# Kernel optimization log

Hardware: AMD Instinct MI355X
Metric: run time of the kernel (lower is better)

The kernel has to match this reference:

```python
import jax, jax.numpy as jnp
import numpy as np

TEMP_POS = 5.0
TEMP_NEG = 10.0
MAX_NEG = 64  # original subsamples at most 64 negatives per row via randperm


def setup_inputs() -> dict:
    key = jax.random.key(0)
    k1, k2 = jax.random.split(key)
    hidden_vectors = jax.random.normal(k1, (1024, 512), dtype=jnp.float32)
    labels = jax.random.randint(k2, (1024,), 0, 2, dtype=jnp.int32)
    return {"hidden_vectors": hidden_vectors, "labels": labels}


def reference(hidden_vectors, labels):
    f32 = hidden_vectors.dtype
    n = hidden_vectors.shape[0]
    # L2-normalize rows, cosine similarity matrix
    h = hidden_vectors / jnp.linalg.norm(hidden_vectors, axis=1, keepdims=True)
    sim = h @ h.T  # (N, N)

    eq = labels[:, None] == labels[None, :]
    eye = jnp.eye(n, dtype=bool)
    mask_pos = eq & ~eye          # same label, not self
    mask_neg = ~eq                # different label

    # Random subsample of up to MAX_NEG negatives per row (Gumbel-free: uniform
    # scores on negative slots, -inf elsewhere, take top-k => uniform random subset).
    noise = jax.random.uniform(jax.random.key(1), (n, n))
    scores = jnp.where(mask_neg, noise, -jnp.inf)
    _, neg_idx = jax.lax.top_k(scores, MAX_NEG)                 # (N, K)
    neg_valid = jnp.take_along_axis(mask_neg, neg_idx, axis=1)  # (N, K) bool
    neg_sim = jnp.take_along_axis(sim, neg_idx, axis=1) / TEMP_NEG  # (N, K)

    pos_sim = sim / TEMP_POS  # (N, N), masked by mask_pos below

    # -log(e^a / (e^a + e^b)) = softplus(b - a)
    pair = jax.nn.softplus(neg_sim[:, None, :] - pos_sim[:, :, None])  # (N, N, K)
    w = mask_pos.astype(f32)[:, :, None] * neg_valid.astype(f32)[:, None, :]
    row_sum = jnp.sum(pair * w, axis=(1, 2))                    # (N,)

    n_pos = jnp.sum(mask_pos, axis=1)
    n_neg = jnp.sum(neg_valid, axis=1)
    n_pairs = (n_pos * n_neg).astype(f32)
    has_pos = n_pos > 0
    row_loss = jnp.where(has_pos, row_sum / jnp.maximum(n_pairs, 1.0), 0.0)

    count = jnp.sum(has_pos).astype(f32)
    return jnp.where(count > 0, jnp.sum(row_loss) / jnp.maximum(count, 1.0), 0.0)
```

## Files before the change

### kernel.cpp

```cpp
#include <hip/hip_runtime.h>
#include <hip/hip_bf16.h>
#include <math.h>
#include <stdint.h>

#define N 1024
#define D 512
#define MAXNEG 64
#define HALF_CNT (1u << 19)

typedef __attribute__((ext_vector_type(8))) short short8;
typedef __attribute__((ext_vector_type(4))) float f32x4;

__device__ __forceinline__ uint32_t rotl32(uint32_t x, uint32_t r) {
    return (x << r) | (x >> (32u - r));
}

__device__ __forceinline__ uint2 tf_pair(uint32_t f) {
    const uint32_t K0 = 0u, K1 = 1u;
    const uint32_t KS2 = 0x1BD11BDBu;
    uint32_t x0 = f, x1 = f + HALF_CNT;
    x0 += K0; x1 += K1;
#define TFR(r) { x0 += x1; x1 = rotl32(x1, (r)); x1 ^= x0; }
    TFR(13) TFR(15) TFR(26) TFR(6)
    x0 += K1;  x1 += KS2 + 1u;
    TFR(17) TFR(29) TFR(16) TFR(24)
    x0 += KS2; x1 += K0 + 2u;
    TFR(13) TFR(15) TFR(26) TFR(6)
    x0 += K0;  x1 += K1 + 3u;
    TFR(17) TFR(29) TFR(16) TFR(24)
    x0 += K1;  x1 += KS2 + 4u;
    TFR(13) TFR(15) TFR(26) TFR(6)
    x0 += KS2; x1 += K0 + 5u;
#undef TFR
    return make_uint2(x0, x1);
}

__device__ __forceinline__ unsigned long long shflx_u64(unsigned long long v, int m) {
    unsigned lo = (unsigned)(v & 0xffffffffull);
    unsigned hi = (unsigned)(v >> 32);
    lo = __shfl_xor(lo, m, 64);
    hi = __shfl_xor(hi, m, 64);
    return ((unsigned long long)hi << 32) | (unsigned long long)lo;
}

__device__ __forceinline__ ushort f2bf(float x) {
    __hip_bfloat16 h = __float2bfloat16(x);
    return *(ushort*)&h;
}

__global__ __launch_bounds__(256) void k_norms(const float* __restrict__ V,
                                               float* __restrict__ inv,
                                               ushort* __restrict__ Vh,
                                               float* __restrict__ gsum,
                                               float* __restrict__ gcnt,
                                               unsigned* __restrict__ done) {
    if (blockIdx.x == 0 && threadIdx.x == 0) { *gsum = 0.0f; *gcnt = 0.0f; *done = 0u; }
    const int w = threadIdx.x >> 6, l = threadIdx.x & 63;
    const int r = blockIdx.x * 4 + w;
    const float4* vp = (const float4*)(V + (size_t)r * D);
    float4 a = vp[l], b = vp[l + 64];
    float ss = a.x*a.x + a.y*a.y + a.z*a.z + a.w*a.w
             + b.x*b.x + b.y*b.y + b.z*b.z + b.w*b.w;
#pragma unroll
    for (int off = 32; off > 0; off >>= 1) ss += __shfl_xor(ss, off, 64);
    if (l == 0) inv[r] = 1.0f / sqrtf(ss);
    ushort4 ua, ub;
    ua.x = f2bf(a.x); ua.y = f2bf(a.y); ua.z = f2bf(a.z); ua.w = f2bf(a.w);
    ub.x = f2bf(b.x); ub.y = f2bf(b.y); ub.z = f2bf(b.z); ub.w = f2bf(b.w);
    *(ushort4*)(Vh + (size_t)r * D + 4 * l)       = ua;
    *(ushort4*)(Vh + (size_t)r * D + 256 + 4 * l) = ub;
}

__global__ __launch_bounds__(64) void k_gemm(const ushort* __restrict__ Vh,
                                             float* __restrict__ sim) {
    const int l  = threadIdx.x;
    const int bi = blockIdx.y, bj = blockIdx.x;
    const int lr = l & 15, lk = (l >> 4) * 8;

    const ushort* Ab = Vh + (size_t)(bi * 64 + lr) * D + lk;
    const ushort* Bb = Vh + (size_t)(bj * 64 + lr) * D + lk;

    f32x4 acc[4][4];
#pragma unroll
    for (int m = 0; m < 4; ++m)
#pragma unroll
        for (int n = 0; n < 4; ++n) acc[m][n] = (f32x4){0.f, 0.f, 0.f, 0.f};

    short8 a[4], b[4], na[4], nb[4];
#pragma unroll
    for (int m = 0; m < 4; ++m) a[m] = *(const short8*)(Ab + (size_t)m * 16 * D);
#pragma unroll
    for (int n = 0; n < 4; ++n) b[n] = *(const short8*)(Bb + (size_t)n * 16 * D);

    for (int k0 = 32; k0 <= D; k0 += 32) {
        if (k0 < D) {
#pragma unroll
            for (int m = 0; m < 4; ++m) na[m] = *(const short8*)(Ab + (size_t)m * 16 * D + k0);
#pragma unroll
            for (int n = 0; n < 4; ++n) nb[n] = *(const short8*)(Bb + (size_t)n * 16 * D + k0);
        }
#pragma unroll
        for (int m = 0; m < 4; ++m)
#pragma unroll
            for (int n = 0; n < 4; ++n)
                acc[m][n] = __builtin_amdgcn_mfma_f32_16x16x32_bf16(a[m], b[n], acc[m][n], 0, 0, 0);
        if (k0 < D) {
#pragma unroll
            for (int m = 0; m < 4; ++m) a[m] = na[m];
#pragma unroll
            for (int n = 0; n < 4; ++n) b[n] = nb[n];
        }
    }

    const int r0 = (l >> 4) * 4;
#pragma unroll
    for (int m = 0; m < 4; ++m) {
#pragma unroll
        for (int r = 0; r < 4; ++r) {
            float* dst = sim + (size_t)(bi * 64 + m * 16 + r0 + r) * N + bj * 64 + lr;
#pragma unroll
            for (int n = 0; n < 4; ++n) dst[n * 16] = acc[m][n][r];
        }
    }
}

__global__ __launch_bounds__(256) void k_rowloss(const float* __restrict__ sim,
                                                 const float* __restrict__ inv,
                                                 const int* __restrict__ labels,
                                                 float* __restrict__ gsum,
                                                 float* __restrict__ gcnt,
                                                 unsigned* __restrict__ done,
                                                 float* __restrict__ out) {
    __shared__ __align__(16) float simrow0[N];
    __shared__ __align__(16) float simrow1[N];
    __shared__ int   hist0[256], hist1[256];
    __shared__ unsigned long long list0[256], list1[256];
    __shared__ float ens0[MAXNEG], ens1[MAXNEG];
    __shared__ int   wpart0[4], wpart1[4];
    __shared__ float wsA[4], wsB[4];
    __shared__ int   wpA[4], wpB[4];
    __shared__ int   s_B0, s_r0, s_cnt0, s_lcnt0;
    __shared__ int   s_B1, s_r1, s_cnt1, s_lcnt1;

    const int b = blockIdx.x;
    const int i0 = b, i1 = b + 512;
    const int t = threadIdx.x;
    const int lane = t & 63, w = t >> 6;
    const int jb = t * 4;

    if (t == 0) {
        s_B0 = -1; s_r0 = 0; s_cnt0 = 0; s_lcnt0 = 0;
        s_B1 = -1; s_r1 = 0; s_cnt1 = 0; s_lcnt1 = 0;
    }
    hist0[t] = 0; hist1[t] = 0;

    {
        const float invi0 = inv[i0], invi1 = inv[i1];
        float4 s0 = ((const float4*)(sim + (size_t)i0 * N))[t];
        float4 s1 = ((const float4*)(sim + (size_t)i1 * N))[t];
        float4 iv = ((const float4*)inv)[t];
        s0.x *= invi0 * iv.x; s0.y *= invi0 * iv.y;
        s0.z *= invi0 * iv.z; s0.w *= invi0 * iv.w;
        s1.x *= invi1 * iv.x; s1.y *= invi1 * iv.y;
        s1.z *= invi1 * iv.z; s1.w *= invi1 * iv.w;
        ((float4*)simrow0)[t] = s0;
        ((float4*)simrow1)[t] = s1;
    }
    const int labi0 = labels[i0], labi1 = labels[i1];
    int4 lv = ((const int4*)labels)[t];
    const int ljs[4] = {lv.x, lv.y, lv.z, lv.w};

    int npos0 = 0, npos1 = 0;
    unsigned long long kq0[4], kq1[4];
    __syncthreads();
#pragma unroll
    for (int q = 0; q < 4; ++q) {
        const int j = jb + q;
        const uint2 rb = tf_pair((uint32_t)(i0 * N + j));
        const bool eq0 = (ljs[q] == labi0), eq1 = (ljs[q] == labi1);
        npos0 += (eq0 && j != i0) ? 1 : 0;
        npos1 += (eq1 && j != i1) ? 1 : 0;
        unsigned long long key0 = 0ull, key1 = 0ull;
        if (!eq0) {
            key0 = ((unsigned long long)(rb.x >> 9) << 11)
                 | (unsigned long long)(2047 - j);
            atomicAdd(&hist0[(int)(key0 >> 26)], 1);
        }
        if (!eq1) {
            key1 = ((unsigned long long)(rb.y >> 9) << 11)
                 | (unsigned long long)(2047 - j);
            atomicAdd(&hist1[(int)(key1 >> 26)], 1);
        }
        kq0[q] = key0; kq1[q] = key1;
    }
    __syncthreads();

    {
        const int own0 = hist0[255 - t], own1 = hist1[255 - t];
        int v0 = own0, v1 = own1;
#pragma unroll
        for (int off = 1; off < 64; off <<= 1) {
            const int u0 = __shfl_up(v0, off, 64);
            const int u1 = __shfl_up(v1, off, 64);
            if (lane >= off) { v0 += u0; v1 += u1; }
        }
        if (lane == 63) { wpart0[w] = v0; wpart1[w] = v1; }
        __syncthreads();
        int add0 = 0, add1 = 0;
#pragma unroll
        for (int k = 0; k < 4; ++k) {
            add0 += (k < w) ? wpart0[k] : 0;
            add1 += (k < w) ? wpart1[k] : 0;
        }
        v0 += add0; v1 += add1;
        if (v0 >= MAXNEG && v0 - own0 < MAXNEG) { s_B0 = 255 - t; s_r0 = MAXNEG - (v0 - own0); }
        if (v1 >= MAXNEG && v1 - own1 < MAXNEG) { s_B1 = 255 - t; s_r1 = MAXNEG - (v1 - own1); }
    }
    __syncthreads();

    const int B0 = s_B0, B1 = s_B1;
#pragma unroll
    for (int q = 0; q < 4; ++q) {
        const unsigned long long key0 = kq0[q], key1 = kq1[q];
        if (key0 != 0ull) {
            const int bk = (int)(key0 >> 26);
            if (bk > B0) {
                const int slot = atomicAdd(&s_cnt0, 1);
                ens0[slot] = __expf(simrow0[2047 - (int)(key0 & 2047ull)] / 10.0f);
            } else if (bk == B0) {
                const int slot = atomicAdd(&s_lcnt0, 1);
                if (slot < 256) list0[slot] = key0;
            }
        }
        if (key1 != 0ull) {
            const int bk = (int)(key1 >> 26);
            if (bk > B1) {
                const int slot = atomicAdd(&s_cnt1, 1);
                ens1[slot] = __expf(simrow1[2047 - (int)(key1 & 2047ull)] / 10.0f);
            } else if (bk == B1) {
                const int slot = atomicAdd(&s_lcnt1, 1);
                if (slot < 256) list1[slot] = key1;
            }
        }
    }
    __syncthreads();

    if (w < 2) {
        const int rr = (w == 0) ? s_r0 : s_r1;
        if (rr > 0) {
            const unsigned long long* lst = (w == 0) ? list0 : list1;
            const int   m    = min((w == 0) ? s_lcnt0 : s_lcnt1, 256);
            const int   base = (w == 0) ? s_cnt0 : s_cnt1;
            float*      ensw = (w == 0) ? ens0 : ens1;
            const float* srw = (w == 0) ? simrow0 : simrow1;
            unsigned long long lk[4];
#pragma unroll
            for (int q = 0; q < 4; ++q) {
                const int idx = lane + q * 64;
                lk[q] = (idx < m) ? lst[idx] : 0ull;
            }
            for (int it = 0; it < rr; ++it) {
                unsigned long long mx = lk[0];
#pragma unroll
                for (int q = 1; q < 4; ++q) mx = lk[q] > mx ? lk[q] : mx;
#pragma unroll
                for (int off = 1; off < 64; off <<= 1) {
                    const unsigned long long o = shflx_u64(mx, off);
                    mx = o > mx ? o : mx;
                }
#pragma unroll
                for (int q = 0; q < 4; ++q) if (lk[q] == mx) lk[q] = 0ull;
                if (lane == 0)
                    ensw[base + it] = __expf(srw[2047 - (int)(mx & 2047ull)] / 10.0f);
            }
        }
    }
    __syncthreads();
    const int nneg0 = s_cnt0 + s_r0;
    const int nneg1 = s_cnt1 + s_r1;

    float ei0[4], ei1[4];
#pragma unroll
    for (int q = 0; q < 4; ++q) {
        const int j = jb + q;
        ei0[q] = (ljs[q] == labi0 && j != i0) ? __expf(-simrow0[j] / 5.0f) : 0.0f;
        ei1[q] = (ljs[q] == labi1 && j != i1) ? __expf(-simrow1[j] / 5.0f) : 0.0f;
    }
    float p00 = 1.0f, p01 = 1.0f, p02 = 1.0f, p03 = 1.0f;
#pragma unroll 8
    for (int k = 0; k < nneg0; ++k) {
        const float e = ens0[k];
        p00 *= fmaf(e, ei0[0], 1.0f);
        p01 *= fmaf(e, ei0[1], 1.0f);
        p02 *= fmaf(e, ei0[2], 1.0f);
        p03 *= fmaf(e, ei0[3], 1.0f);
    }
    float p10 = 1.0f, p11 = 1.0f, p12 = 1.0f, p13 = 1.0f;
#pragma unroll 8
    for (int k = 0; k < nneg1; ++k) {
        const float e = ens1[k];
        p10 *= fmaf(e, ei1[0], 1.0f);
        p11 *= fmaf(e, ei1[1], 1.0f);
        p12 *= fmaf(e, ei1[2], 1.0f);
        p13 *= fmaf(e, ei1[3], 1.0f);
    }
    float r0 = __logf(p00) + __logf(p01) + __logf(p02) + __logf(p03);
    float r1 = __logf(p10) + __logf(p11) + __logf(p12) + __logf(p13);

#pragma unroll
    for (int off = 32; off > 0; off >>= 1) {
        r0 += __shfl_xor(r0, off, 64);
        r1 += __shfl_xor(r1, off, 64);
        npos0 += __shfl_xor(npos0, off, 64);
        npos1 += __shfl_xor(npos1, off, 64);
    }
    if (lane == 0) { wsA[w] = r0; wsB[w] = r1; wpA[w] = npos0; wpB[w] = npos1; }
    __syncthreads();
    if (t == 0) {
        const float rs0 = wsA[0] + wsA[1] + wsA[2] + wsA[3];
        const float rs1 = wsB[0] + wsB[1] + wsB[2] + wsB[3];
        const int   np0 = wpA[0] + wpA[1] + wpA[2] + wpA[3];
        const int   np1 = wpB[0] + wpB[1] + wpB[2] + wpB[3];
        const float rl0 = (np0 > 0) ? rs0 / fmaxf((float)np0 * (float)nneg0, 1.0f) : 0.0f;
        const float rl1 = (np1 > 0) ? rs1 / fmaxf((float)np1 * (float)nneg1, 1.0f) : 0.0f;
        const float hp  = (np0 > 0 ? 1.0f : 0.0f) + (np1 > 0 ? 1.0f : 0.0f);
        atomicAdd(gsum, rl0 + rl1);
        atomicAdd(gcnt, hp);
        __threadfence();
        const unsigned old = atomicAdd(done, 1u);
        if (old == (N / 2) - 1) {
            const float Sv = atomicAdd(gsum, 0.0f);
            const float Cv = atomicAdd(gcnt, 0.0f);
            out[0] = (Cv > 0.0f) ? Sv / fmaxf(Cv, 1.0f) : 0.0f;
        }
    }
}

extern "C" void kernel_launch(void* const* d_in, const int* in_sizes, int n_in,
                              void* d_out, int out_size, void* d_ws, size_t ws_size,
                              hipStream_t stream) {
    const float* V      = (const float*)d_in[0];
    const int*   labels = (const int*)d_in[1];
    float* out = (float*)d_out;

    char* ws = (char*)d_ws;
    float*    inv  = (float*)(ws);
    float*    gsum = (float*)(ws + 4096);
    float*    gcnt = (float*)(ws + 4096 + 16);
    unsigned* done = (unsigned*)(ws + 4096 + 32);
    ushort*   Vh   = (ushort*)(ws + 8192);
    float*    sim  = (float*)(ws + 8192 + 1048576);

    k_norms  <<<N / 4, 256, 0, stream>>>(V, inv, Vh, gsum, gcnt, done);
    k_gemm   <<<dim3(N / 64, N / 64), 64, 0, stream>>>(Vh, sim);
    k_rowloss<<<N / 2, 256, 0, stream>>>(sim, inv, labels, gsum, gcnt, done, out);
}
```

Before: 97.26 us.

## Fuse row-norm and bf16 conversion into GEMM, use four-wave blocks

Removes the separate norm/convert kernel: the GEMM now reads fp32 rows directly, converts them to bf16 fragments in registers, and takes the inverse norms from the diagonal of the diagonal tiles (the bf16 self dot product). Each 64x64 tile is now split across four waves holding 32x32 sub-tiles instead of one wave, which raises parallelism. The intent is to save one launch and the round trip of the bf16 copy through memory. In exchange, global reads are doubled (fp32 instead of bf16), every tile converts its operands again, and the norms are now computed from bf16-rounded values, which changes the numerics slightly.

```diff
diff --git a/kernel.cpp b/kernel.cpp
--- a/kernel.cpp
+++ b/kernel.cpp
@@ -48,78 +48,97 @@
     return *(ushort*)&h;
 }
 
-__global__ __launch_bounds__(256) void k_norms(const float* __restrict__ V,
-                                               float* __restrict__ inv,
-                                               ushort* __restrict__ Vh,
-                                               float* __restrict__ gsum,
-                                               float* __restrict__ gcnt,
-                                               unsigned* __restrict__ done) {
-    if (blockIdx.x == 0 && threadIdx.x == 0) { *gsum = 0.0f; *gcnt = 0.0f; *done = 0u; }
-    const int w = threadIdx.x >> 6, l = threadIdx.x & 63;
-    const int r = blockIdx.x * 4 + w;
-    const float4* vp = (const float4*)(V + (size_t)r * D);
-    float4 a = vp[l], b = vp[l + 64];
-    float ss = a.x*a.x + a.y*a.y + a.z*a.z + a.w*a.w
-             + b.x*b.x + b.y*b.y + b.z*b.z + b.w*b.w;
-#pragma unroll
-    for (int off = 32; off > 0; off >>= 1) ss += __shfl_xor(ss, off, 64);
-    if (l == 0) inv[r] = 1.0f / sqrtf(ss);
-    ushort4 ua, ub;
-    ua.x = f2bf(a.x); ua.y = f2bf(a.y); ua.z = f2bf(a.z); ua.w = f2bf(a.w);
-    ub.x = f2bf(b.x); ub.y = f2bf(b.y); ub.z = f2bf(b.z); ub.w = f2bf(b.w);
-    *(ushort4*)(Vh + (size_t)r * D + 4 * l)       = ua;
-    *(ushort4*)(Vh + (size_t)r * D + 256 + 4 * l) = ub;
-}
-
-__global__ __launch_bounds__(64) void k_gemm(const ushort* __restrict__ Vh,
-                                             float* __restrict__ sim) {
-    const int l  = threadIdx.x;
+__device__ __forceinline__ short8 to_frag(float4 a, float4 b) {
+    short8 r;
+    r[0] = (short)f2bf(a.x); r[1] = (short)f2bf(a.y);
+    r[2] = (short)f2bf(a.z); r[3] = (short)f2bf(a.w);
+    r[4] = (short)f2bf(b.x); r[5] = (short)f2bf(b.y);
+    r[6] = (short)f2bf(b.z); r[7] = (short)f2bf(b.w);
+    return r;
+}
+
+__global__ __launch_bounds__(256) void k_gemm(const float* __restrict__ V,
+                                              float* __restrict__ sim,
+                                              float* __restrict__ inv,
+                                              float* __restrict__ gsum,
+                                              float* __restrict__ gcnt,
+                                              unsigned* __restrict__ done) {
+    if (blockIdx.x == 0 && blockIdx.y == 0 && threadIdx.x == 0) {
+        *gsum = 0.0f; *gcnt = 0.0f; *done = 0u;
+    }
+    const int t  = threadIdx.x;
+    const int w  = t >> 6, l = t & 63;
+    const int wr = w >> 1, wc = w & 1;
+    const int lr = l & 15, lk = (l >> 4) * 8;
     const int bi = blockIdx.y, bj = blockIdx.x;
-    const int lr = l & 15, lk = (l >> 4) * 8;
-
-    const ushort* Ab = Vh + (size_t)(bi * 64 + lr) * D + lk;
-    const ushort* Bb = Vh + (size_t)(bj * 64 + lr) * D + lk;
-
-    f32x4 acc[4][4];
-#pragma unroll
-    for (int m = 0; m < 4; ++m)
-#pragma unroll
-        for (int n = 0; n < 4; ++n) acc[m][n] = (f32x4){0.f, 0.f, 0.f, 0.f};
-
-    short8 a[4], b[4], na[4], nb[4];
-#pragma unroll
-    for (int m = 0; m < 4; ++m) a[m] = *(const short8*)(Ab + (size_t)m * 16 * D);
-#pragma unroll
-    for (int n = 0; n < 4; ++n) b[n] = *(const short8*)(Bb + (size_t)n * 16 * D);
-
-    for (int k0 = 32; k0 <= D; k0 += 32) {
-        if (k0 < D) {
-#pragma unroll
-            for (int m = 0; m < 4; ++m) na[m] = *(const short8*)(Ab + (size_t)m * 16 * D + k0);
-#pragma unroll
-            for (int n = 0; n < 4; ++n) nb[n] = *(const short8*)(Bb + (size_t)n * 16 * D + k0);
-        }
-#pragma unroll
-        for (int m = 0; m < 4; ++m)
-#pragma unroll
-            for (int n = 0; n < 4; ++n)
+
+    const float* A0 = V + (size_t)(bi * 64 + wr * 32 + lr) * D + lk;
+    const float* B0 = V + (size_t)(bj * 64 + wc * 32 + lr) * D + lk;
+
+    f32x4 acc[2][2];
+#pragma unroll
+    for (int m = 0; m < 2; ++m)
+#pragma unroll
+        for (int n = 0; n < 2; ++n) acc[m][n] = (f32x4){0.f, 0.f, 0.f, 0.f};
+
+    float4 cA[2][2], cB[2][2];
+#pragma unroll
+    for (int m = 0; m < 2; ++m) {
+        cA[m][0] = *(const float4*)(A0 + (size_t)m * 16 * D);
+        cA[m][1] = *(const float4*)(A0 + (size_t)m * 16 * D + 4);
+        cB[m][0] = *(const float4*)(B0 + (size_t)m * 16 * D);
+        cB[m][1] = *(const float4*)(B0 + (size_t)m * 16 * D + 4);
+    }
+
+    for (int k0 = 0; k0 < D; k0 += 32) {
+        const bool more = (k0 + 32) < D;
+        float4 nA[2][2], nB[2][2];
+        if (more) {
+#pragma unroll
+            for (int m = 0; m < 2; ++m) {
+                nA[m][0] = *(const float4*)(A0 + (size_t)m * 16 * D + k0 + 32);
+                nA[m][1] = *(const float4*)(A0 + (size_t)m * 16 * D + k0 + 36);
+                nB[m][0] = *(const float4*)(B0 + (size_t)m * 16 * D + k0 + 32);
+                nB[m][1] = *(const float4*)(B0 + (size_t)m * 16 * D + k0 + 36);
+            }
+        }
+        short8 a[2], b[2];
+#pragma unroll
+        for (int m = 0; m < 2; ++m) {
+            a[m] = to_frag(cA[m][0], cA[m][1]);
+            b[m] = to_frag(cB[m][0], cB[m][1]);
+        }
+#pragma unroll
+        for (int m = 0; m < 2; ++m)
+#pragma unroll
+            for (int n = 0; n < 2; ++n)
                 acc[m][n] = __builtin_amdgcn_mfma_f32_16x16x32_bf16(a[m], b[n], acc[m][n], 0, 0, 0);
-        if (k0 < D) {
-#pragma unroll
-            for (int m = 0; m < 4; ++m) a[m] = na[m];
-#pragma unroll
-            for (int n = 0; n < 4; ++n) b[n] = nb[n];
+        if (more) {
+#pragma unroll
+            for (int m = 0; m < 2; ++m) {
+                cA[m][0] = nA[m][0]; cA[m][1] = nA[m][1];
+                cB[m][0] = nB[m][0]; cB[m][1] = nB[m][1];
+            }
         }
     }
 
     const int r0 = (l >> 4) * 4;
 #pragma unroll
-    for (int m = 0; m < 4; ++m) {
+    for (int m = 0; m < 2; ++m) {
 #pragma unroll
         for (int r = 0; r < 4; ++r) {
-            float* dst = sim + (size_t)(bi * 64 + m * 16 + r0 + r) * N + bj * 64 + lr;
-#pragma unroll
-            for (int n = 0; n < 4; ++n) dst[n * 16] = acc[m][n][r];
+            const int grow = bi * 64 + wr * 32 + m * 16 + r0 + r;
+            float* dst = sim + (size_t)grow * N + bj * 64 + wc * 32 + lr;
+            dst[0]  = acc[m][0][r];
+            dst[16] = acc[m][1][r];
+        }
+    }
+    if (bi == bj && wr == wc && (lr >> 2) == (l >> 4)) {
+        const int r = lr & 3;
+#pragma unroll
+        for (int m = 0; m < 2; ++m) {
+            const int grow = bi * 64 + wr * 32 + m * 16 + r0 + r;
+            inv[grow] = 1.0f / sqrtf(acc[m][m][r]);
         }
     }
 }
@@ -348,10 +367,8 @@
     float*    gsum = (float*)(ws + 4096);
     float*    gcnt = (float*)(ws + 4096 + 16);
     unsigned* done = (unsigned*)(ws + 4096 + 32);
-    ushort*   Vh   = (ushort*)(ws + 8192);
-    float*    sim  = (float*)(ws + 8192 + 1048576);
-
-    k_norms  <<<N / 4, 256, 0, stream>>>(V, inv, Vh, gsum, gcnt, done);
-    k_gemm   <<<dim3(N / 64, N / 64), 64, 0, stream>>>(Vh, sim);
+    float*    sim  = (float*)(ws + 8192);
+
+    k_gemm   <<<dim3(N / 64, N / 64), 256, 0, stream>>>(V, sim, inv, gsum, gcnt, done);
     k_rowloss<<<N / 2, 256, 0, stream>>>(sim, inv, labels, gsum, gcnt, done, out);
 }
```

After: 100.2 us. 1.03x slower.
